# Performance work log

Hardware: AMD Instinct MI355X
Metric: run time of the kernel (lower is better)

## Reference

```python
import jax, jax.numpy as jnp
import numpy as np

B, S, H, E, I, K = 1, 4096, 1024, 16, 512, 2
ISH = 1024  # shared expert intermediate = moe_intermediate_size * num_shared_experts
ROUTE_SCALE = 1.0
WSCALE = 0.02


def setup_inputs() -> dict:
    key = jax.random.key(0)
    ks = jax.random.split(key, 9)
    return {
        "hidden_states": jax.random.normal(ks[0], (B, S, H), dtype=jnp.float32),
        "router_w": jax.random.normal(ks[1], (H, E), dtype=jnp.float32) * WSCALE,
        "expert_bias": jnp.zeros((E,), dtype=jnp.float32),
        "w_gate": jax.random.normal(ks[2], (E, H, I), dtype=jnp.float32) * WSCALE,
        "w_up": jax.random.normal(ks[3], (E, H, I), dtype=jnp.float32) * WSCALE,
        "w_down": jax.random.normal(ks[4], (E, I, H), dtype=jnp.float32) * WSCALE,
        "sw_gate": jax.random.normal(ks[5], (H, ISH), dtype=jnp.float32) * WSCALE,
        "sw_up": jax.random.normal(ks[6], (H, ISH), dtype=jnp.float32) * WSCALE,
        "sw_down": jax.random.normal(ks[7], (ISH, H), dtype=jnp.float32) * WSCALE,
    }


def reference(hidden_states, router_w, expert_bias, w_gate, w_up, w_down, sw_gate, sw_up, sw_down):
    b, s, h = hidden_states.shape
    T = b * s
    xf = hidden_states.reshape(T, h)

    # --- token-choice router (sigmoid scores, top-k, normalize, scale) ---
    scores = jax.nn.sigmoid((xf @ router_w).astype(jnp.float32))          # [T, E]
    _, sel = jax.lax.top_k(scores + expert_bias[None, :], K)              # [T, K] int32
    top = jnp.take_along_axis(scores, sel, axis=1)                        # [T, K]
    top = top / (top.sum(axis=-1, keepdims=True) + 1e-20)
    top = top * ROUTE_SCALE

    # combine weights: [T, E], zero for unselected experts
    comb = jnp.zeros((T, E), jnp.float32).at[jnp.arange(T)[:, None], sel].add(top)

    # --- routed experts: SwiGLU MLP per expert (stacked weights) ---
    g = jnp.einsum('th,ehi->eti', xf, w_gate)                             # [E, T, I]
    u = jnp.einsum('th,ehi->eti', xf, w_up)                               # [E, T, I]
    a = jax.nn.silu(g) * u                                                # [E, T, I]
    eo = jnp.einsum('eti,eih->eth', a, w_down)                            # [E, T, H]
    routed = jnp.einsum('eth,te->th', eo.astype(jnp.float32), comb).astype(hidden_states.dtype)

    # --- shared experts (always active) ---
    shared = (jax.nn.silu(xf @ sw_gate) * (xf @ sw_up)) @ sw_down         # [T, H]

    return (shared + routed).reshape(b, s, h)
```

## Files before the change

### kernel.cpp

```cpp
#include <hip/hip_runtime.h>
#include <math.h>

#define T_TOK 4096
#define HDIM  1024
#define NEXP  16
#define IDIM  512
#define NSLOT 16384
#define NGRP  18
#define MAXRB 80

typedef unsigned int u32;
typedef unsigned short u16;
typedef __attribute__((ext_vector_type(8))) short bfrag;
typedef __attribute__((ext_vector_type(4))) float f32x4;

__device__ __forceinline__ u16 f2bf(float f) {
    union { float f; u32 u; } c; c.f = f;
    u32 u = c.u;
    u32 r = u + 0x7fffu + ((u >> 16) & 1u);
    return (u16)(r >> 16);
}
__device__ __forceinline__ float bf2f(u16 h) {
    union { u32 u; float f; } c; c.u = ((u32)h) << 16;
    return c.f;
}

__device__ __forceinline__ void async16(void* lds, const void* g) {
    __builtin_amdgcn_global_load_lds((__attribute__((address_space(1))) void*)(g),
                                     (__attribute__((address_space(3))) void*)(lds),
                                     16, 0, 0);
}

#define VMW(n) asm volatile("s_waitcnt vmcnt(" #n ")" ::: "memory")
#define BARSB() do { __builtin_amdgcn_s_barrier(); __builtin_amdgcn_sched_barrier(0); } while (0)
#define SB0()   __builtin_amdgcn_sched_barrier(0)

__global__ __launch_bounds__(256) void cvt_f32_bf16(const float* __restrict__ src,
                                                    u16* __restrict__ dst, int n) {
    int i = (blockIdx.x * 256 + threadIdx.x) * 4;
    if (i >= n) return;
    float4 v = *(const float4*)(src + i);
    ushort4 o;
    o.x = f2bf(v.x); o.y = f2bf(v.y); o.z = f2bf(v.z); o.w = f2bf(v.w);
    *(ushort4*)(dst + i) = o;
}

__global__ __launch_bounds__(256) void transpose_k2(const float* __restrict__ src,
                                                    u16* __restrict__ dst,
                                                    int R, int C, long bstride) {
    __shared__ u16 tileT[32][132];
    long base = (long)blockIdx.z * bstride;
    int c0 = blockIdx.x * 32, r0 = blockIdx.y * 128;
    int t = threadIdx.x;
    int rr = t >> 3;
    int c4 = (t & 7) * 4;
#pragma unroll
    for (int p = 0; p < 4; ++p) {
        int r = p * 32 + rr;
        float4 v = *(const float4*)(src + base + (long)(r0 + r) * C + c0 + c4);
        tileT[c4 + 0][r] = f2bf(v.x);
        tileT[c4 + 1][r] = f2bf(v.y);
        tileT[c4 + 2][r] = f2bf(v.z);
        tileT[c4 + 3][r] = f2bf(v.w);
    }
    __syncthreads();
    int cc = t >> 5;
    int r4 = (t & 31) * 4;
#pragma unroll
    for (int q = 0; q < 4; ++q) {
        int c = q * 8 + cc;
        ushort4 o;
        o.x = tileT[c][r4]; o.y = tileT[c][r4 + 1];
        o.z = tileT[c][r4 + 2]; o.w = tileT[c][r4 + 3];
        *(ushort4*)(dst + base + (long)(c0 + c) * R + r0 + r4) = o;
    }
}

__global__ __launch_bounds__(256) void router_k(const float* __restrict__ x,
                                                const float* __restrict__ rw,
                                                const float* __restrict__ bias,
                                                int* __restrict__ sel,
                                                float* __restrict__ wts) {
    int tid = threadIdx.x;
    int wv = tid >> 6;
    int lane = tid & 63;
    int t = blockIdx.x * 4 + wv;
    int e = lane & 15, hc = lane >> 4;
    const float* xr = x + (long)t * HDIM + hc * 256;
    const float* rp = rw + (long)hc * 256 * NEXP + e;
    float acc = 0.f;
#pragma unroll 4
    for (int i = 0; i < 64; ++i) {
        float4 xv = *(const float4*)(xr + i * 4);
        acc += xv.x * rp[(i * 4 + 0) * NEXP] + xv.y * rp[(i * 4 + 1) * NEXP]
             + xv.z * rp[(i * 4 + 2) * NEXP] + xv.w * rp[(i * 4 + 3) * NEXP];
    }
    acc += __shfl_down(acc, 16);
    acc += __shfl_down(acc, 32);
    float sc = 1.f / (1.f + __expf(-acc));
    float v = sc + bias[e];
    int i0 = -1, i1 = -1;
    float v0 = -1e30f, v1 = -1e30f, s0 = 0.f, s1 = 0.f;
#pragma unroll
    for (int j = 0; j < 16; ++j) {
        float vj = __shfl(v, j);
        float scj = __shfl(sc, j);
        if (vj > v0) { v1 = v0; i1 = i0; s1 = s0; v0 = vj; i0 = j; s0 = scj; }
        else if (vj > v1) { v1 = vj; i1 = j; s1 = scj; }
    }
    if (lane == 0) {
        float nrm = s0 + s1 + 1e-20f;
        sel[t * 2] = i0; sel[t * 2 + 1] = i1;
        wts[t * 2] = s0 / nrm; wts[t * 2 + 1] = s1 / nrm;
    }
}

__global__ __launch_bounds__(1024) void route_build_k(const int* __restrict__ sel,
                                                      int* __restrict__ offs,
                                                      int* __restrict__ rowmap,
                                                      int* __restrict__ invmap,
                                                      int* __restrict__ rbGroup,
                                                      int* __restrict__ rbRow0) {
    __shared__ int hist[NEXP];
    __shared__ int cur[NEXP];
    int tid = threadIdx.x;
    if (tid < NEXP) hist[tid] = 0;
    __syncthreads();
    for (int i = tid; i < T_TOK * 2; i += 1024)
        atomicAdd(&hist[sel[i]], 1);
    __syncthreads();
    if (tid == 0) {
        int a = 0;
        for (int g = 0; g < NEXP; ++g) { cur[g] = a; offs[g] = a; a += hist[g]; }
        offs[16] = 8192;
        offs[17] = 8192 + T_TOK;
        offs[18] = 8192 + 2 * T_TOK;
        int rb = 0;
        for (int g = 0; g < NGRP; ++g)
            for (int r0 = offs[g]; r0 < offs[g + 1]; r0 += 256) {
                rbGroup[rb] = g; rbRow0[rb] = r0; ++rb;
            }
        for (; rb < MAXRB; ++rb) rbGroup[rb] = -1;
    }
    __syncthreads();
    for (int i = tid; i < T_TOK * 2; i += 1024) {
        int g = sel[i];
        int slot = atomicAdd(&cur[g], 1);
        rowmap[slot] = i >> 1;
        invmap[i] = slot;
    }
    for (int i = tid; i < T_TOK; i += 1024) {
        rowmap[8192 + i] = i;
        rowmap[8192 + T_TOK + i] = i;
    }
}

__global__ __launch_bounds__(512)
void gemm_gu(const u16* __restrict__ A,
             const u16* __restrict__ WG,
             const u16* __restrict__ WU,
             const u16* __restrict__ SWG,
             const u16* __restrict__ SWU,
             u16* __restrict__ H,
             const int* __restrict__ offs,
             const int* __restrict__ rowmap,
             const int* __restrict__ rbGroup,
             const int* __restrict__ rbRow0) {
    const int NWG = 4 * MAXRB;
    int f = blockIdx.x;
    int L = (f & 7) * (NWG / 8) + (f >> 3);
    int cb = L & 3;
    int rb = L >> 2;
    int g = rbGroup[rb];
    if (g < 0) return;
    int row0 = rbRow0[rb];
    int mend = offs[g + 1];
    int col0 = cb * 128;
    long wb = (long)((g < 16) ? g : (g - 16)) * IDIM * HDIM;
    const u16* Bg = (g < 16) ? WG + wb : SWG + wb;
    const u16* Bu = (g < 16) ? WU + wb : SWU + wb;

    __shared__ u16 sA[2][256 * 64];
    __shared__ u16 sBg[2][128 * 64];
    __shared__ u16 sBu[2][128 * 64];

    int tid = threadIdx.x;
    int lane = tid & 63;
    int w = tid >> 6;
    int wr = (w >> 1) * 64;
    int wc = (w & 1) * 64;
    int lhi = lane >> 4, llo = lane & 15;
    int swz = llo & 7;

    const u16* pA[4]; int dA[4];
#pragma unroll
    for (int c = 0; c < 4; ++c) {
        int idx = c * 512 + tid;
        int r = idx >> 3, ch = idx & 7;
        int grow = row0 + r;
        int ar = rowmap[(grow < mend) ? grow : row0];
        pA[c] = A + (long)ar * HDIM + ((ch ^ (r & 7)) * 8);
        dA[c] = idx * 8;
    }
    const u16* pBg[2]; const u16* pBu[2]; int dB[2];
#pragma unroll
    for (int c = 0; c < 2; ++c) {
        int idx = c * 512 + tid;
        int r = idx >> 3, ch = idx & 7;
        long boff = (long)(col0 + r) * HDIM + ((ch ^ (r & 7)) * 8);
        pBg[c] = Bg + boff; pBu[c] = Bu + boff;
        dB[c] = idx * 8;
    }

    f32x4 accg[4][4], accu[4][4];
#pragma unroll
    for (int m = 0; m < 4; ++m)
#pragma unroll
        for (int n = 0; n < 4; ++n) {
            f32x4 z = {0.f, 0.f, 0.f, 0.f};
            accg[m][n] = z; accu[m][n] = z;
        }

    auto STAGE_A = [&](int buf) {
#pragma unroll
        for (int c = 0; c < 4; ++c) { async16(&sA[buf][dA[c]], pA[c]); pA[c] += 64; }
    };
    auto STAGE_GU = [&](int buf) {
#pragma unroll
        for (int c = 0; c < 2; ++c) {
            async16(&sBg[buf][dB[c]], pBg[c]); pBg[c] += 64;
            async16(&sBu[buf][dB[c]], pBu[c]); pBu[c] += 64;
        }
    };

    bfrag av[4], bv[4];
    auto RD_A = [&](int buf, int kk) {
        int p = ((kk * 4 + lhi) ^ swz) * 8;
#pragma unroll
        for (int m = 0; m < 4; ++m)
            av[m] = *(const bfrag*)&sA[buf][(wr + m * 16 + llo) * 64 + p];
    };
    auto RD_BG = [&](int buf, int kk) {
        int p = ((kk * 4 + lhi) ^ swz) * 8;
#pragma unroll
        for (int n = 0; n < 4; ++n)
            bv[n] = *(const bfrag*)&sBg[buf][(wc + n * 16 + llo) * 64 + p];
    };
    auto RD_BU = [&](int buf, int kk) {
        int p = ((kk * 4 + lhi) ^ swz) * 8;
#pragma unroll
        for (int n = 0; n < 4; ++n)
            bv[n] = *(const bfrag*)&sBu[buf][(wc + n * 16 + llo) * 64 + p];
    };
    auto MM = [&](f32x4 (&ac)[4][4]) {
        __builtin_amdgcn_s_setprio(1);
#pragma unroll
        for (int m = 0; m < 4; ++m)
#pragma unroll
            for (int n = 0; n < 4; ++n)
                ac[m][n] = __builtin_amdgcn_mfma_f32_16x16x32_bf16(av[m], bv[n], ac[m][n], 0, 0, 0);
        __builtin_amdgcn_s_setprio(0);
        __builtin_amdgcn_sched_barrier(0);
    };

    const int NT = HDIM / 64;
    STAGE_A(0); STAGE_GU(0);
#pragma unroll 1
    for (int t = 0; t < NT - 1; ++t) {
        int cur = t & 1, nxt = cur ^ 1;
        STAGE_A(nxt);
        VMW(4); BARSB();
        RD_A(cur, 0); RD_BG(cur, 0); MM(accg);
        STAGE_GU(nxt);
        BARSB();
        RD_BU(cur, 0); MM(accu);
        BARSB();
        RD_A(cur, 1); RD_BG(cur, 1); MM(accg);
        BARSB();
        RD_BU(cur, 1); MM(accu);
    }
    {
        int cur = (NT - 1) & 1;
        VMW(0); BARSB();
        RD_A(cur, 0); RD_BG(cur, 0); MM(accg);
        RD_BU(cur, 0); MM(accu);
        RD_A(cur, 1); RD_BG(cur, 1); MM(accg);
        RD_BU(cur, 1); MM(accu);
    }

#pragma unroll
    for (int m = 0; m < 4; ++m) {
        int rbase = row0 + wr + m * 16 + lhi * 4;
#pragma unroll
        for (int n = 0; n < 4; ++n) {
            int col = col0 + wc + n * 16 + llo;
#pragma unroll
            for (int i = 0; i < 4; ++i) {
                int grow = rbase + i;
                if (grow >= mend) continue;
                float gv = accg[m][n][i], uv = accu[m][n][i];
                float hv = gv / (1.f + __expf(-gv)) * uv;
                H[(long)grow * IDIM + col] = f2bf(hv);
            }
        }
    }
}

__global__ __launch_bounds__(512)
void gemm_down(const u16* __restrict__ Hbuf,
               const u16* __restrict__ WD,
               const u16* __restrict__ SWD,
               u16* __restrict__ EO,
               const int* __restrict__ offs,
               const int* __restrict__ rbGroup,
               const int* __restrict__ rbRow0) {
    const int NWG = 4 * MAXRB;
    int f = blockIdx.x;
    int L = (f & 7) * (NWG / 8) + (f >> 3);
    int cb = L & 3;
    int rb = L >> 2;
    int g = rbGroup[rb];
    if (g < 0) return;
    int row0 = rbRow0[rb];
    int mend = offs[g + 1];
    int col0 = cb * 256;
    long wb = (long)((g < 16) ? g : (g - 16)) * HDIM * IDIM;
    const u16* B = (g < 16) ? WD + wb : SWD + wb;

    __shared__ u16 sA[2][256 * 64];
    __shared__ u16 sB[2][256 * 64];

    int tid = threadIdx.x;
    int lane = tid & 63;
    int w = tid >> 6;
    int wr = (w >> 2) * 128;
    int wc = (w & 3) * 64;
    int lhi = lane >> 4, llo = lane & 15;
    int swz = llo & 7;

    const u16* pA[4]; const u16* pB[4]; int dd[4];
#pragma unroll
    for (int c = 0; c < 4; ++c) {
        int idx = c * 512 + tid;
        int r = idx >> 3, ch = idx & 7;
        int grow = row0 + r;
        int ar = (grow < mend) ? grow : row0;
        int chs = (ch ^ (r & 7)) * 8;
        pA[c] = Hbuf + (long)ar * IDIM + chs;
        pB[c] = B + (long)(col0 + r) * IDIM + chs;
        dd[c] = idx * 8;
    }

    f32x4 acc[8][4];
#pragma unroll
    for (int m = 0; m < 8; ++m)
#pragma unroll
        for (int n = 0; n < 4; ++n) { f32x4 z = {0.f, 0.f, 0.f, 0.f}; acc[m][n] = z; }

    auto STAGE_A = [&](int buf) {
#pragma unroll
        for (int c = 0; c < 4; ++c) { async16(&sA[buf][dd[c]], pA[c]); pA[c] += 64; }
    };
    auto STAGE_B = [&](int buf) {
#pragma unroll
        for (int c = 0; c < 4; ++c) { async16(&sB[buf][dd[c]], pB[c]); pB[c] += 64; }
    };

    bfrag av[4], bb[4];
    auto RD_A = [&](int buf, int kk, int ro) {
        int p = ((kk * 4 + lhi) ^ swz) * 8;
#pragma unroll
        for (int m = 0; m < 4; ++m)
            av[m] = *(const bfrag*)&sA[buf][(wr + ro + m * 16 + llo) * 64 + p];
    };
    auto RD_B = [&](int buf, int kk) {
        int p = ((kk * 4 + lhi) ^ swz) * 8;
#pragma unroll
        for (int n = 0; n < 4; ++n)
            bb[n] = *(const bfrag*)&sB[buf][(wc + n * 16 + llo) * 64 + p];
    };
    auto MMD = [&](int mo) {
        __builtin_amdgcn_s_setprio(1);
#pragma unroll
        for (int m = 0; m < 4; ++m)
#pragma unroll
            for (int n = 0; n < 4; ++n)
                acc[mo + m][n] = __builtin_amdgcn_mfma_f32_16x16x32_bf16(av[m], bb[n], acc[mo + m][n], 0, 0, 0);
        __builtin_amdgcn_s_setprio(0);
        __builtin_amdgcn_sched_barrier(0);
    };

    const int NT = IDIM / 64;
    STAGE_B(0); STAGE_A(0);
#pragma unroll 1
    for (int t = 0; t < NT - 1; ++t) {
        int cur = t & 1, nxt = cur ^ 1;
        STAGE_B(nxt);
        VMW(4); BARSB();
        RD_A(cur, 0, 0); RD_B(cur, 0); MMD(0);
        STAGE_A(nxt);
        BARSB();
        RD_A(cur, 0, 64); MMD(4);
        BARSB();
        RD_A(cur, 1, 0); RD_B(cur, 1); MMD(0);
        BARSB();
        RD_A(cur, 1, 64); MMD(4);
    }
    {
        int cur = (NT - 1) & 1;
        VMW(0); BARSB();
        RD_A(cur, 0, 0); RD_B(cur, 0); MMD(0);
        RD_A(cur, 0, 64); MMD(4);
        RD_A(cur, 1, 0); RD_B(cur, 1); MMD(0);
        RD_A(cur, 1, 64); MMD(4);
    }

#pragma unroll
    for (int m = 0; m < 8; ++m) {
        int rbase = row0 + wr + m * 16 + lhi * 4;
#pragma unroll
        for (int n = 0; n < 4; ++n) {
            int col = col0 + wc + n * 16 + llo;
#pragma unroll
            for (int i = 0; i < 4; ++i) {
                int grow = rbase + i;
                if (grow >= mend) continue;
                EO[(long)grow * HDIM + col] = f2bf(acc[m][n][i]);
            }
        }
    }
}

__global__ __launch_bounds__(256) void combine_k(float* __restrict__ out,
                                                 const u16* __restrict__ eo,
                                                 const int* __restrict__ invmap,
                                                 const float* __restrict__ wts) {
    int t = blockIdx.x;
    int h = threadIdx.x * 4;
    int r0 = invmap[t * 2], r1 = invmap[t * 2 + 1];
    float w0 = wts[t * 2], w1 = wts[t * 2 + 1];
    int s0 = 8192 + t, s1 = 8192 + T_TOK + t;
    ushort4 a = *(const ushort4*)(eo + (long)r0 * HDIM + h);
    ushort4 b = *(const ushort4*)(eo + (long)r1 * HDIM + h);
    ushort4 c = *(const ushort4*)(eo + (long)s0 * HDIM + h);
    ushort4 d = *(const ushort4*)(eo + (long)s1 * HDIM + h);
    float4 o;
    o.x = w0 * bf2f(a.x) + w1 * bf2f(b.x) + bf2f(c.x) + bf2f(d.x);
    o.y = w0 * bf2f(a.y) + w1 * bf2f(b.y) + bf2f(c.y) + bf2f(d.y);
    o.z = w0 * bf2f(a.z) + w1 * bf2f(b.z) + bf2f(c.z) + bf2f(d.z);
    o.w = w0 * bf2f(a.w) + w1 * bf2f(b.w) + bf2f(c.w) + bf2f(d.w);
    *(float4*)(out + (long)t * HDIM + h) = o;
}

extern "C" void kernel_launch(void* const* d_in, const int* in_sizes, int n_in,
                              void* d_out, int out_size, void* d_ws, size_t ws_size,
                              hipStream_t stream) {
    const float* x    = (const float*)d_in[0];
    const float* rw   = (const float*)d_in[1];
    const float* bias = (const float*)d_in[2];
    const float* wg   = (const float*)d_in[3];
    const float* wu   = (const float*)d_in[4];
    const float* wd   = (const float*)d_in[5];
    const float* swg  = (const float*)d_in[6];
    const float* swu  = (const float*)d_in[7];
    const float* swd  = (const float*)d_in[8];
    float* out = (float*)d_out;

    char* ws = (char*)d_ws;
    size_t o = 0;
    auto alloc = [&](size_t bytes) -> void* {
        void* p = ws + o;
        o += (bytes + 255) & ~(size_t)255;
        return p;
    };
    u16* x_bf = (u16*)alloc((size_t)T_TOK * HDIM * 2);
    u16* WtG  = (u16*)alloc((size_t)NEXP * IDIM * HDIM * 2);
    u16* WtU  = (u16*)alloc((size_t)NEXP * IDIM * HDIM * 2);
    u16* WtD  = (u16*)alloc((size_t)NEXP * HDIM * IDIM * 2);
    u16* SWtG = (u16*)alloc((size_t)2 * IDIM * HDIM * 2);
    u16* SWtU = (u16*)alloc((size_t)2 * IDIM * HDIM * 2);
    u16* SWtD = (u16*)alloc((size_t)2 * HDIM * IDIM * 2);
    u16* Hbuf = (u16*)alloc((size_t)NSLOT * IDIM * 2);
    int*   sel     = (int*)alloc((size_t)T_TOK * 2 * 4);
    float* wts     = (float*)alloc((size_t)T_TOK * 2 * 4);
    int*   invmap  = (int*)alloc((size_t)T_TOK * 2 * 4);
    int*   rowmap  = (int*)alloc((size_t)NSLOT * 4);
    int*   offs    = (int*)alloc((NGRP + 1) * 4);
    int*   rbGroup = (int*)alloc(MAXRB * 4);
    int*   rbRow0  = (int*)alloc(MAXRB * 4);
    u16* EO = WtG;

    cvt_f32_bf16<<<dim3((T_TOK * HDIM) / (4 * 256)), 256, 0, stream>>>(x, x_bf, T_TOK * HDIM);

    transpose_k2<<<dim3(IDIM / 32, HDIM / 128, NEXP), 256, 0, stream>>>(wg, WtG, HDIM, IDIM, (long)HDIM * IDIM);
    transpose_k2<<<dim3(IDIM / 32, HDIM / 128, NEXP), 256, 0, stream>>>(wu, WtU, HDIM, IDIM, (long)HDIM * IDIM);
    transpose_k2<<<dim3(HDIM / 32, IDIM / 128, NEXP), 256, 0, stream>>>(wd, WtD, IDIM, HDIM, (long)IDIM * HDIM);
    transpose_k2<<<dim3((2 * IDIM) / 32, HDIM / 128, 1), 256, 0, stream>>>(swg, SWtG, HDIM, 2 * IDIM, 0);
    transpose_k2<<<dim3((2 * IDIM) / 32, HDIM / 128, 1), 256, 0, stream>>>(swu, SWtU, HDIM, 2 * IDIM, 0);
    transpose_k2<<<dim3(HDIM / 32, IDIM / 128, 2), 256, 0, stream>>>(swd, SWtD, IDIM, HDIM, (long)IDIM * HDIM);

    router_k<<<dim3(T_TOK / 4), 256, 0, stream>>>(x, rw, bias, sel, wts);
    route_build_k<<<dim3(1), 1024, 0, stream>>>(sel, offs, rowmap, invmap, rbGroup, rbRow0);

    gemm_gu<<<dim3(4 * MAXRB), 512, 0, stream>>>(
        x_bf, WtG, WtU, SWtG, SWtU, Hbuf, offs, rowmap, rbGroup, rbRow0);

    gemm_down<<<dim3(4 * MAXRB), 512, 0, stream>>>(
        Hbuf, WtD, SWtD, EO, offs, rbGroup, rbRow0);

    combine_k<<<dim3(T_TOK), 256, 0, stream>>>(out, EO, invmap, wts);
}
```

Baseline: 192.2 us.

## Restructure GEMM main loops into barrier-separated LDS-read and MFMA phases

Result: no change. 188.9 us (-1.7%).

```diff
diff --git a/kernel.cpp b/kernel.cpp
--- a/kernel.cpp
+++ b/kernel.cpp
@@ -33,7 +33,6 @@
 
 #define VMW(n) asm volatile("s_waitcnt vmcnt(" #n ")" ::: "memory")
 #define BARSB() do { __builtin_amdgcn_s_barrier(); __builtin_amdgcn_sched_barrier(0); } while (0)
-#define SB0()   __builtin_amdgcn_sched_barrier(0)
 
 __global__ __launch_bounds__(256) void cvt_f32_bf16(const float* __restrict__ src,
                                                     u16* __restrict__ dst, int n) {
@@ -265,27 +264,30 @@
 
     const int NT = HDIM / 64;
     STAGE_A(0); STAGE_GU(0);
+    VMW(0); BARSB();
 #pragma unroll 1
-    for (int t = 0; t < NT - 1; ++t) {
+    for (int t = 0; t < NT; ++t) {
         int cur = t & 1, nxt = cur ^ 1;
-        STAGE_A(nxt);
-        VMW(4); BARSB();
-        RD_A(cur, 0); RD_BG(cur, 0); MM(accg);
-        STAGE_GU(nxt);
-        BARSB();
-        RD_BU(cur, 0); MM(accu);
-        BARSB();
-        RD_A(cur, 1); RD_BG(cur, 1); MM(accg);
-        BARSB();
-        RD_BU(cur, 1); MM(accu);
-    }
-    {
-        int cur = (NT - 1) & 1;
-        VMW(0); BARSB();
-        RD_A(cur, 0); RD_BG(cur, 0); MM(accg);
-        RD_BU(cur, 0); MM(accu);
-        RD_A(cur, 1); RD_BG(cur, 1); MM(accg);
-        RD_BU(cur, 1); MM(accu);
+        bool pf = (t < NT - 1);
+        RD_A(cur, 0); RD_BG(cur, 0);
+        if (pf) STAGE_A(nxt);
+        BARSB();
+        MM(accg);
+        BARSB();
+        RD_BU(cur, 0);
+        if (pf) STAGE_GU(nxt);
+        BARSB();
+        MM(accu);
+        BARSB();
+        RD_A(cur, 1); RD_BG(cur, 1);
+        BARSB();
+        MM(accg);
+        BARSB();
+        RD_BU(cur, 1);
+        BARSB();
+        MM(accu);
+        if (pf) VMW(0);
+        BARSB();
     }
 
 #pragma unroll
@@ -392,27 +394,30 @@
 
     const int NT = IDIM / 64;
     STAGE_B(0); STAGE_A(0);
+    VMW(0); BARSB();
 #pragma unroll 1
-    for (int t = 0; t < NT - 1; ++t) {
+    for (int t = 0; t < NT; ++t) {
         int cur = t & 1, nxt = cur ^ 1;
-        STAGE_B(nxt);
-        VMW(4); BARSB();
-        RD_A(cur, 0, 0); RD_B(cur, 0); MMD(0);
-        STAGE_A(nxt);
-        BARSB();
-        RD_A(cur, 0, 64); MMD(4);
-        BARSB();
-        RD_A(cur, 1, 0); RD_B(cur, 1); MMD(0);
-        BARSB();
-        RD_A(cur, 1, 64); MMD(4);
-    }
-    {
-        int cur = (NT - 1) & 1;
-        VMW(0); BARSB();
-        RD_A(cur, 0, 0); RD_B(cur, 0); MMD(0);
-        RD_A(cur, 0, 64); MMD(4);
-        RD_A(cur, 1, 0); RD_B(cur, 1); MMD(0);
-        RD_A(cur, 1, 64); MMD(4);
+        bool pf = (t < NT - 1);
+        RD_A(cur, 0, 0); RD_B(cur, 0);
+        if (pf) STAGE_B(nxt);
+        BARSB();
+        MMD(0);
+        BARSB();
+        RD_A(cur, 0, 64);
+        if (pf) STAGE_A(nxt);
+        BARSB();
+        MMD(4);
+        BARSB();
+        RD_A(cur, 1, 0); RD_B(cur, 1);
+        BARSB();
+        MMD(0);
+        BARSB();
+        RD_A(cur, 1, 64);
+        BARSB();
+        MMD(4);
+        if (pf) VMW(0);
+        BARSB();
     }
 
 #pragma unroll
```
